# Performance work log

Measured on AMD Instinct MI355X. Metric: run time of the kernel, lower is better.

Reference implementation:

```python
import jax, jax.numpy as jnp
import numpy as np
from jax import lax

DG = 8          # deformable groups
KH = KW = 3
K = KH * KW
PAD = 1


def conv3x3(x, w, b):
    # x: (B,C,H,W), w: (O,C,3,3) -> SAME conv, stride 1
    y = lax.conv_general_dilated(x, w, (1, 1), ((PAD, PAD), (PAD, PAD)),
                                 dimension_numbers=('NCHW', 'OIHW', 'NCHW'))
    return y + b[None, :, None, None]


def lrelu(x):
    return jnp.where(x >= 0, x, 0.1 * x)


def modulated_deform_conv(x, offset, mask, w, b):
    """DCNv2 semantics: stride=1, pad=1, dilation=1, groups=1.
    x: (B,C,H,W); offset: (B, 2*DG*K, H, W); mask: (B, DG*K, H, W) (already sigmoided);
    w: (O, C, 3, 3); b: (O,).
    Offset channel layout per CUDA kernel: (DG, K, 2[y,x]).
    """
    B, C, H, W = x.shape
    cg = C // DG
    off = offset.reshape(B, DG, K, 2, H, W)
    dy, dx = off[:, :, :, 0], off[:, :, :, 1]            # (B,DG,K,H,W)

    ky, kx = jnp.meshgrid(jnp.arange(KH), jnp.arange(KW), indexing='ij')
    ky = ky.reshape(K).astype(x.dtype)
    kx = kx.reshape(K).astype(x.dtype)
    base_y = jnp.arange(H, dtype=x.dtype)[None, :, None] - PAD + ky[:, None, None]  # (K,H,1)
    base_x = jnp.arange(W, dtype=x.dtype)[None, None, :] - PAD + kx[:, None, None]  # (K,1,W)
    py = dy + base_y                                     # (B,DG,K,H,W)
    px = dx + base_x

    y0 = jnp.floor(py)
    x0 = jnp.floor(px)
    wy = py - y0
    wx = px - x0
    y0i = y0.astype(jnp.int32)
    x0i = x0.astype(jnp.int32)

    xg = x.reshape(B, DG, cg, H * W)

    def gather(yi, xi):
        valid = ((yi >= 0) & (yi < H) & (xi >= 0) & (xi < W)).astype(x.dtype)
        idx = jnp.clip(yi, 0, H - 1) * W + jnp.clip(xi, 0, W - 1)   # (B,DG,K,H,W)
        idxf = idx.reshape(B, DG, 1, K * H * W)
        vals = jnp.take_along_axis(xg, jnp.broadcast_to(idxf, (B, DG, cg, K * H * W)), axis=3)
        return vals.reshape(B, DG, cg, K, H, W) * valid[:, :, None]

    samp = gather(y0i, x0i) * ((1 - wy) * (1 - wx))[:, :, None]
    samp = samp + gather(y0i, x0i + 1) * ((1 - wy) * wx)[:, :, None]
    samp = samp + gather(y0i + 1, x0i) * (wy * (1 - wx))[:, :, None]
    samp = samp + gather(y0i + 1, x0i + 1) * (wy * wx)[:, :, None]

    samp = samp * mask.reshape(B, DG, 1, K, H, W)        # modulated
    wr = w.reshape(w.shape[0], DG, cg, K)
    out = jnp.einsum('odck,bdckhw->bohw', wr, samp)
    return out + b[None, :, None, None]


def dcn_pack(x, feat, off_w, off_b, w, b):
    # conv_offset on `feat` -> (B, 3*DG*K, H, W); chunk into o1,o2,mask
    out = conv3x3(feat, off_w, off_b)
    o1, o2, m = jnp.split(out, 3, axis=1)
    offset = jnp.concatenate([o1, o2], axis=1)
    mask = jax.nn.sigmoid(m)
    return modulated_deform_conv(x, offset, mask, w, b)


def setup_inputs() -> dict:
    key = jax.random.key(0)
    ks = jax.random.split(key, 24)
    B, C, H, W = 4, 64, 192, 192
    nf = C

    def wconv(k, o, i, s=0.02):
        return jax.random.normal(k, (o, i, 3, 3), jnp.float32) * s

    inp = {
        'nbr_l1': jax.random.normal(ks[0], (B, C, H, W), jnp.float32),
        'ref_l1': jax.random.normal(ks[1], (B, C, H, W), jnp.float32),
        'oc1_w': wconv(ks[2], nf, 2 * nf), 'oc1_b': jnp.zeros((nf,), jnp.float32),
        'oc2_w': wconv(ks[3], nf, nf), 'oc2_b': jnp.zeros((nf,), jnp.float32),
        'dcn1_off_w': wconv(ks[4], 3 * DG * K, nf, 0.01), 'dcn1_off_b': jnp.zeros((3 * DG * K,), jnp.float32),
        'dcn1_w': wconv(ks[5], nf, nf), 'dcn1_b': jnp.zeros((nf,), jnp.float32),
        'fc_w': wconv(ks[6], nf, nf), 'fc_b': jnp.zeros((nf,), jnp.float32),
        'cas1_w': wconv(ks[7], nf, 2 * nf), 'cas1_b': jnp.zeros((nf,), jnp.float32),
        'cas2_w': wconv(ks[8], nf, nf), 'cas2_b': jnp.zeros((nf,), jnp.float32),
        'casd_off_w': wconv(ks[9], 3 * DG * K, nf, 0.01), 'casd_off_b': jnp.zeros((3 * DG * K,), jnp.float32),
        'casd_w': wconv(ks[10], nf, nf), 'casd_b': jnp.zeros((nf,), jnp.float32),
    }
    return inp


def reference(nbr_l1, ref_l1, oc1_w, oc1_b, oc2_w, oc2_b,
              dcn1_off_w, dcn1_off_b, dcn1_w, dcn1_b, fc_w, fc_b,
              cas1_w, cas1_b, cas2_w, cas2_b,
              casd_off_w, casd_off_b, casd_w, casd_b):
    offset = jnp.concatenate([nbr_l1, ref_l1], axis=1)
    offset = lrelu(conv3x3(offset, oc1_w, oc1_b))
    offset = lrelu(conv3x3(offset, oc2_w, oc2_b))
    feat = dcn_pack(nbr_l1, offset, dcn1_off_w, dcn1_off_b, dcn1_w, dcn1_b)
    feat = conv3x3(feat, fc_w, fc_b)                     # no activation (matches source)
    offset = jnp.concatenate([feat, ref_l1], axis=1)
    offset = lrelu(conv3x3(lrelu(conv3x3(offset, cas1_w, cas1_b)), cas2_w, cas2_b))
    feat = lrelu(dcn_pack(feat, offset, casd_off_w, casd_off_b, casd_w, casd_b))
    return feat
```

## Files before the change

### kernel.cpp

```cpp
#include <hip/hip_runtime.h>
#include <hip/hip_bf16.h>
#include <math.h>

typedef __hip_bfloat16 bf16;
typedef float  floatx16 __attribute__((ext_vector_type(16)));
typedef short  short8   __attribute__((ext_vector_type(8)));

#define Bn 4
#define NF 64
#define Hn 192
#define Wn 192
#define HWn (Hn*Wn)

#define WA_OC1  0
#define WA_OC2  73728
#define WA_FC   110592
#define WA_CAS1 147456
#define WA_CAS2 221184
#define WA_D1O  258048
#define WA_CDO  405504
#define WP_D1   552960
#define WP_CD   589824
#define B_OC1  0
#define B_OC2  64
#define B_FC   128
#define B_CAS1 192
#define B_CAS2 256
#define B_D1O  320
#define B_CDO  536
#define B_D1P  752
#define B_CDP  816
#define BIAS_OFF  1024
#define WPOOL_OFF 5120
#define BUF_OFF   1261568
#define FEAT_BYTES 18874368

#define WROWS 12
#define WCOLS 12
#define WSTR  72
#define SSTR2 152

__device__ __forceinline__ float b2f(bf16 v){ return __bfloat162float(v); }
__device__ __forceinline__ bf16  f2b(float v){ return __float2bfloat16(v); }
__device__ __forceinline__ float us2f(unsigned short u){ return __uint_as_float(((unsigned)u) << 16); }
__device__ __forceinline__ float ld(const void* p, size_t i, int f32){
    if (f32) return ((const float*)p)[i];
    return b2f(((const bf16*)p)[i]);
}

union B8 { uint2 u2[2]; uint4 u4; short8 s8; };
union V8 { uint4 u4; unsigned short us[8]; bf16 h[8]; };
union V4 { uint2 u2; bf16 h[4]; };

struct P20 { const void* p[20]; int n[20]; };

__global__ void detect_bias(P20 a, int* __restrict__ flags, float* __restrict__ bp){
    __shared__ int sf[20];
    int t = threadIdx.x;
    if (t < 20){
        const unsigned short* u = (const unsigned short*)a.p[t];
        int n = a.n[t]; if (n > 512) n = 512;
        int f32 = 0;
        for (int i = 0; i < n; ++i){
            float v = __uint_as_float(((unsigned)u[i]) << 16);
            if (!(fabsf(v) < 1e3f)) f32 = 1;
        }
        sf[t] = f32; flags[t] = f32;
    }
    __syncthreads();
    const int src[9] = {3,5,11,13,15,7,17,9,19};
    const int off[9] = {B_OC1,B_OC2,B_FC,B_CAS1,B_CAS2,B_D1O,B_CDO,B_D1P,B_CDP};
    const int sz[9]  = {64,64,64,64,64,216,216,64,64};
    for (int s = 0; s < 9; ++s)
        if (t < sz[s]) bp[off[s] + t] = ld(a.p[src[s]], t, sf[src[s]]);
}

__global__ void prep_weights(P20 a, const int* __restrict__ flags, bf16* __restrict__ wp)
{
    const int srcI[9] = {2,4,10,12,14,6,16,8,18};
    const int dstO[9] = {WA_OC1,WA_OC2,WA_FC,WA_CAS1,WA_CAS2,WA_D1O,WA_CDO,WP_D1,WP_CD};
    const int cinA[9] = {128,64,64,128,64,64,64,0,0};
    const int coutA[9]= {64,64,64,64,64,216,216,0,0};
    const int nblk[9] = {288,144,144,288,144,576,576,144,144};

    int bx = blockIdx.x;
    int j = 0, base = 0;
    while (j < 8 && bx >= base + nblk[j]){ base += nblk[j]; ++j; }
    int idx = (bx - base)*256 + threadIdx.x;
    const void* src = a.p[srcI[j]];
    const int f = flags[srcI[j]];
    bf16* dst = wp + dstO[j];

    int jj = idx & 7;
    int ko = (idx>>3) & 1;
    int mm = (idx>>4) & 31;
    int rest = idx >> 9;
    if (cinA[j]){
        int KK = cinA[j] >> 4;
        int kk = rest % KK; rest /= KK;
        int tap = rest % 9;
        int ocb = rest / 9;
        int oc = ocb*32 + mm;
        int ci = kk*16 + ko*8 + jj;
        float v = 0.f;
        if (oc < coutA[j]) v = ld(src, ((size_t)oc*cinA[j] + ci)*9 + tap, f);
        dst[idx] = f2b(v);
    } else {
        int kk = rest % 36;
        int ocb = rest / 36;
        int oc = ocb*32 + mm;
        int kp   = kk*16 + ko*8 + jj;
        int slot = kp >> 3;
        int cg   = kp & 7;
        int dg   = slot / 9;
        int tap  = slot - dg*9;
        int k    = (dg*8 + cg)*9 + tap;
        dst[idx] = f2b(ld(src, (size_t)oc*576 + k, f));
    }
}

__global__ __launch_bounds__(256)
void pack_x(const void* __restrict__ src, const int* __restrict__ flags, int fi,
            bf16* __restrict__ dst)
{
    __shared__ bf16 s[64*65];
    const int b    = blockIdx.y;
    const int pix0 = blockIdx.x * 64;
    const int t    = threadIdx.x;
    const int f    = (fi >= 0) ? flags[fi] : 0;

    const int px8 = (t & 7) * 8;
    const int ci0 = t >> 3;
#pragma unroll
    for (int it = 0; it < 2; ++it){
        int ci = ci0 + it*32;
        size_t g = ((size_t)b*NF + ci)*HWn + pix0 + px8;
        if (f){
            float4 a0 = *(const float4*)((const float*)src + g);
            float4 a1 = *(const float4*)((const float*)src + g + 4);
            bf16* sp = &s[ci*65 + px8];
            sp[0]=f2b(a0.x); sp[1]=f2b(a0.y); sp[2]=f2b(a0.z); sp[3]=f2b(a0.w);
            sp[4]=f2b(a1.x); sp[5]=f2b(a1.y); sp[6]=f2b(a1.z); sp[7]=f2b(a1.w);
        } else {
            V8 v; v.u4 = *(const uint4*)((const bf16*)src + g);
            bf16* sp = &s[ci*65 + px8];
#pragma unroll
            for (int j = 0; j < 8; ++j) sp[j] = v.h[j];
        }
    }
    __syncthreads();

    const int px  = t >> 2;
    const int ch0 = (t & 3) * 16;
    V8 o0, o1;
#pragma unroll
    for (int j = 0; j < 8; ++j){
        o0.h[j] = s[(ch0 + j)*65 + px];
        o1.h[j] = s[(ch0 + 8 + j)*65 + px];
    }
    bf16* dp = dst + ((size_t)b*HWn + pix0 + px)*64 + ch0;
    *(uint4*)(dp)     = o0.u4;
    *(uint4*)(dp + 8) = o1.u4;
}

template<int KK, int NOCB>
__global__ __launch_bounds__(256)
void conv_mfma(const bf16* __restrict__ inA, const bf16* __restrict__ inB,
               const bf16* __restrict__ wA, const float* __restrict__ bias,
               bf16* __restrict__ out, int ACT)
{
    constexpr int CinT  = KK*16;
    constexpr int ciPad = CinT + 4;
    constexpr int CH8   = CinT/8;
    constexpr int CSH   = (KK==4)?3:4;
    extern __shared__ __align__(16) char smem_raw[];
    bf16* s_in = (bf16*)smem_raw;

    const int b  = blockIdx.z;
    const int bx = blockIdx.x;
    const int ty = bx/3, tx = bx - ty*3;
    const int h0 = ty*2, x0 = tx*64;
    const int tid = threadIdx.x;

    for (int r = 0; r < 4; ++r){
        const int y = h0 - 1 + r;
        const bool yv = (unsigned)y < (unsigned)Hn;
        const size_t rb = ((size_t)b*HWn + (size_t)y*Wn)*64;
        for (int e = tid; e < 66*CH8; e += 256){
            const int c   = e >> CSH;
            const int ch8 = e & (CH8-1);
            const int x = x0 - 1 + c;
            B8 v; v.u4 = make_uint4(0,0,0,0);
            if (yv && (unsigned)x < (unsigned)Wn){
                if (KK==8 && ch8 >= 8) v.u4 = *(const uint4*)(inB + rb + (size_t)x*64 + (ch8-8)*8);
                else                   v.u4 = *(const uint4*)(inA + rb + (size_t)x*64 + ch8*8);
            }
            bf16* dp = &s_in[(size_t)(r*66 + c)*ciPad + ch8*8];
            *(uint2*)(dp)     = v.u2[0];
            *(uint2*)(dp + 4) = v.u2[1];
        }
    }
    __syncthreads();

    const int w    = tid >> 6;
    const int lane = tid & 63;
    const int m    = lane & 31;
    const int half = lane >> 5;
    const int och  = (w >> 1) * 32;
    const int rw   = (w & 1);
    const int gpx0 = (h0 + rw)*Wn + x0;

#pragma unroll
    for (int ot = 0; ot < NOCB; ++ot){
        const int ocb = ot*2 + (w >> 1);
        const bf16* wb = wA + ((size_t)ocb*9*KK)*512 + m*16 + half*8;

        floatx16 a0, a1;
#pragma unroll
        for (int r = 0; r < 16; ++r){ a0[r] = 0.f; a1[r] = 0.f; }

        B8 ring[2][4];
#pragma unroll
        for (int i = 0; i < 4; ++i) ring[0][i].u4 = *(const uint4*)(wb + (size_t)i*512);

        constexpr int NCH = 9*KK/4;
#pragma unroll
        for (int tap = 0; tap < 9; ++tap){
            const int ky = tap/3, kx = tap - 3*(tap/3);
            const bf16* s0 = s_in + (size_t)((ky+rw)*66 + kx + m)*ciPad + half*8;
#pragma unroll
            for (int hh = 0; hh < KK/4; ++hh){
                const int cidx = tap*(KK/4) + hh;
                const int cur = cidx & 1, nxt = cur ^ 1;
                if (cidx + 1 < NCH){
#pragma unroll
                    for (int i = 0; i < 4; ++i)
                        ring[nxt][i].u4 = *(const uint4*)(wb + (size_t)((cidx+1)*4 + i)*512);
                }
#pragma unroll
                for (int i = 0; i < 4; ++i){
                    const bf16* p0 = s0 + hh*64 + i*16;
                    const bf16* p1 = p0 + 32*ciPad;
                    B8 b0, b1;
                    b0.u2[0] = *(const uint2*)(p0); b0.u2[1] = *(const uint2*)(p0+4);
                    b1.u2[0] = *(const uint2*)(p1); b1.u2[1] = *(const uint2*)(p1+4);
                    a0 = __builtin_amdgcn_mfma_f32_32x32x16_bf16(ring[cur][i].s8, b0.s8, a0, 0,0,0);
                    a1 = __builtin_amdgcn_mfma_f32_32x32x16_bf16(ring[cur][i].s8, b1.s8, a1, 0,0,0);
                }
            }
        }

        if (ACT == 2){
#pragma unroll
            for (int s = 0; s < 2; ++s){
                const int px = gpx0 + s*32 + m;
#pragma unroll
                for (int r = 0; r < 16; ++r){
                    int row = (r & 3) + 8*(r >> 2) + 4*half;
                    int oc  = ot*64 + och + row;
                    if (oc < 216){
                        float v = (s ? a1[r] : a0[r]) + bias[oc];
                        if (oc >= 144) v = 1.f/(1.f + __expf(-v));
                        out[((size_t)b*216 + oc)*HWn + px] = f2b(v);
                    }
                }
            }
        } else {
#pragma unroll
            for (int s = 0; s < 2; ++s){
                const int px = gpx0 + s*32 + m;
                bf16* ob = out + ((size_t)b*HWn + px)*64 + och + 4*half;
#pragma unroll
                for (int q = 0; q < 4; ++q){
                    V4 u;
#pragma unroll
                    for (int j = 0; j < 4; ++j){
                        float v = (s ? a1[q*4+j] : a0[q*4+j]) + bias[och + 4*half + 8*q + j];
                        if (ACT == 1) v = (v >= 0.f) ? v : 0.1f*v;
                        u.h[j] = f2b(v);
                    }
                    *(uint2*)(ob + 8*q) = u.u2;
                }
            }
        }
    }
}

__global__ __launch_bounds__(256)
void dcn_mfma(const bf16* __restrict__ xi,
              const bf16* __restrict__ offs,
              const bf16* __restrict__ wP,
              const float* __restrict__ pbias,
              void* __restrict__ out, int outF32, int ACT)
{
    __shared__ __align__(16) bf16 s_win[WROWS*WCOLS*WSTR];
    __shared__ __align__(16) bf16 s_samp[64*SSTR2];

    const int b   = blockIdx.y;
    const int bx  = blockIdx.x;
    const int tx  = bx % (Wn/8);
    const int ty  = bx / (Wn/8);
    const int gx0 = tx*8, gy0 = ty*8;
    const int wx0 = gx0 - 2, wy0 = gy0 - 2;
    const int tid = threadIdx.x;

    const bf16* xb = xi + (size_t)b*HWn*64;

    for (int c = tid; c < WROWS*WCOLS*8; c += 256){
        int ch4 = c & 7;
        int pxi = c >> 3;
        int gy  = wy0 + pxi/WCOLS;
        int gx  = wx0 + pxi%WCOLS;
        uint4 v = {0u,0u,0u,0u};
        if ((unsigned)gy < (unsigned)Hn && (unsigned)gx < (unsigned)Wn)
            v = *(const uint4*)(xb + ((size_t)gy*Wn + gx)*64 + ch4*8);
        *(uint4*)&s_win[pxi*WSTR + ch4*8] = v;
    }

    const int px   = tid & 63;
    const int wq   = tid >> 6;
    const int pr   = px >> 3, pc = px & 7;
    const int gy   = gy0 + pr, gx = gx0 + pc;
    const int m    = px & 31;
    const int half = px >> 5;
    const int och  = (wq >> 1) * 32;
    const int pxh  = (wq & 1) * 32;

    const size_t obase = (size_t)b*216*HWn + (size_t)gy*Wn + gx;
    const uint4 z4 = {0u,0u,0u,0u};

    const bf16* wPb  = wP + ((size_t)(wq>>1)*36)*512 + m*16 + half*8;
    const bf16* srow = s_samp + (pxh + m)*SSTR2 + half*8;

    floatx16 acc;
#pragma unroll
    for (int r = 0; r < 16; ++r) acc[r] = 0.f;

    for (int pass = 0; pass < 4; ++pass){
        __syncthreads();

#pragma unroll
        for (int ii = 0; ii < 5; ++ii){
            int sl = wq + ii*4;
            if (sl < 18){
                int dgl = sl / 9;
                int tap = sl - dgl*9;
                int dg  = pass*2 + dgl;
                int ky  = tap / 3;
                int kx  = tap - ky*3;
                float dy = b2f(offs[obase + (size_t)(dg*18 + tap*2    )*HWn]);
                float dx = b2f(offs[obase + (size_t)(dg*18 + tap*2 + 1)*HWn]);
                float mk = b2f(offs[obase + (size_t)(144 + dg*9 + tap )*HWn]);
                float py  = dy + (float)(gy - 1 + ky);
                float pxx = dx + (float)(gx - 1 + kx);
                float y0f = floorf(py), x0f = floorf(pxx);
                int   y0  = (int)y0f,   xi0 = (int)x0f;
                float wy  = py - y0f,   wx  = pxx - x0f;
                float w00 = (1.f-wy)*(1.f-wx)*mk, w01 = (1.f-wy)*wx*mk;
                float w10 = wy*(1.f-wx)*mk,       w11 = wy*wx*mk;
                int ly = y0 - wy0, lx = xi0 - wx0;

                auto fetch = [&](int ly_, int lx_, int y_, int x_) -> uint4 {
                    if ((unsigned)ly_ < (unsigned)WROWS && (unsigned)lx_ < (unsigned)WCOLS)
                        return *(const uint4*)&s_win[(ly_*WCOLS + lx_)*WSTR + dg*8];
                    if ((unsigned)y_ < (unsigned)Hn && (unsigned)x_ < (unsigned)Wn)
                        return *(const uint4*)(xb + ((size_t)y_*Wn + x_)*64 + dg*8);
                    return z4;
                };
                V8 c00, c01, c10, c11, o;
                c00.u4 = fetch(ly,   lx,   y0,   xi0  );
                c01.u4 = fetch(ly,   lx+1, y0,   xi0+1);
                c10.u4 = fetch(ly+1, lx,   y0+1, xi0  );
                c11.u4 = fetch(ly+1, lx+1, y0+1, xi0+1);
#pragma unroll
                for (int j = 0; j < 8; ++j){
                    float v = w00*us2f(c00.us[j]) + w01*us2f(c01.us[j])
                            + w10*us2f(c10.us[j]) + w11*us2f(c11.us[j]);
                    o.h[j] = f2b(v);
                }
                *(uint4*)&s_samp[px*SSTR2 + sl*8] = o.u4;
            }
        }
        __syncthreads();

#pragma unroll
        for (int kk = 0; kk < 9; ++kk){
            B8 ba; ba.u4 = *(const uint4*)(wPb + (size_t)(pass*9 + kk)*512);
            B8 bb; bb.u4 = *(const uint4*)(srow + kk*16);
            acc = __builtin_amdgcn_mfma_f32_32x32x16_bf16(ba.s8, bb.s8, acc, 0, 0, 0);
        }
    }

    const int opx = pxh + m;
    const int pxo = (gy0 + (opx >> 3))*Wn + gx0 + (opx & 7);
    if (outF32){
#pragma unroll
        for (int r = 0; r < 16; ++r){
            int row = (r & 3) + 8*(r >> 2) + 4*half;
            int oc  = och + row;
            float v = acc[r] + pbias[oc];
            if (ACT) v = (v >= 0.f) ? v : 0.1f*v;
            ((float*)out)[((size_t)b*NF + oc)*HWn + pxo] = v;
        }
    } else {
        bf16* ob = (bf16*)out + ((size_t)b*HWn + pxo)*64 + och + 4*half;
#pragma unroll
        for (int q = 0; q < 4; ++q){
            V4 u;
#pragma unroll
            for (int j = 0; j < 4; ++j){
                int oc = och + 4*half + 8*q + j;
                float v = acc[q*4 + j] + pbias[oc];
                if (ACT) v = (v >= 0.f) ? v : 0.1f*v;
                u.h[j] = f2b(v);
            }
            *(uint2*)(ob + 8*q) = u.u2;
        }
    }
}

extern "C" void kernel_launch(void* const* d_in, const int* in_sizes, int n_in,
                              void* d_out, int out_size, void* d_ws, size_t ws_size,
                              hipStream_t stream)
{
    enum { I_NBR=0, I_REF=1 };

    int*   flags = (int*)d_ws;
    float* bp    = (float*)((char*)d_ws + BIAS_OFF);
    bf16*  wp    = (bf16*) ((char*)d_ws + WPOOL_OFF);
    bf16*  t1    = (bf16*) ((char*)d_ws + BUF_OFF);
    bf16*  f1    = (bf16*) ((char*)d_ws + BUF_OFF + FEAT_BYTES);
    bf16*  offs  = (bf16*) ((char*)d_ws + BUF_OFF + 2*(size_t)FEAT_BYTES);
    bf16*  t0    = (bf16*) d_out;
    bf16*  nbr_i = (bf16*)((char*)d_out + FEAT_BYTES);
    bf16*  refA  = offs;
    bf16*  refB  = nbr_i;

    P20 a;
    for (int i = 0; i < 20; ++i){ a.p[i] = d_in[i]; a.n[i] = in_sizes[i]; }

    detect_bias<<<1, 256, 0, stream>>>(a, flags, bp);
    prep_weights<<<2448, 256, 0, stream>>>(a, flags, wp);

    dim3 blk(256,1,1);
    const int smem64  = 4*66*68*2;
    const int smem128 = 4*66*132*2;
    dim3 gC (288, 1, Bn);
    dim3 gD (576, Bn, 1);
    dim3 gP (576, Bn, 1);

    pack_x<<<gP, blk, 0, stream>>>(d_in[I_NBR], flags, I_NBR, nbr_i);
    pack_x<<<gP, blk, 0, stream>>>(d_in[I_REF], flags, I_REF, refA);
    conv_mfma<8,1><<<gC, blk, smem128, stream>>>(nbr_i, refA, wp+WA_OC1, bp+B_OC1, t0, 1);
    conv_mfma<4,1><<<gC, blk, smem64, stream>>>(t0, nullptr, wp+WA_OC2, bp+B_OC2, t1, 1);
    conv_mfma<4,4><<<gC, blk, smem64, stream>>>(t1, nullptr, wp+WA_D1O, bp+B_D1O, offs, 2);
    dcn_mfma<<<gD, blk, 0, stream>>>(nbr_i, offs, wp+WP_D1, bp+B_D1P, t1, 0, 0);
    pack_x<<<gP, blk, 0, stream>>>(d_in[I_REF], flags, I_REF, refB);
    conv_mfma<4,1><<<gC, blk, smem64, stream>>>(t1, nullptr, wp+WA_FC, bp+B_FC, f1, 0);
    conv_mfma<8,1><<<gC, blk, smem128, stream>>>(f1, refB, wp+WA_CAS1, bp+B_CAS1, t0, 1);
    conv_mfma<4,1><<<gC, blk, smem64, stream>>>(t0, nullptr, wp+WA_CAS2, bp+B_CAS2, t1, 1);
    conv_mfma<4,4><<<gC, blk, smem64, stream>>>(t1, nullptr, wp+WA_CDO, bp+B_CDO, offs, 2);
    dcn_mfma<<<gD, blk, 0, stream>>>(f1, offs, wp+WP_CD, bp+B_CDP, d_out, 1, 1);
}
```

Baseline: 862.3 us.

## Process four output rows per block in 64-channel convs to reuse weights

Adds a ROWS template parameter to the MFMA conv kernel so the 64-input-channel convolutions handle 4 output rows per block instead of 2, with each wave keeping 4 accumulators. Each weight fragment loaded from global memory is now reused across twice as many pixel sub-tiles, and the halo overhead in the staged input shrinks relative to output. The cost is more accumulator registers (64 floats), larger shared memory, half as many blocks, and the outer output-tile loop is no longer forced to unroll.

```diff
diff --git a/kernel.cpp b/kernel.cpp
--- a/kernel.cpp
+++ b/kernel.cpp
@@ -163,7 +163,7 @@
     *(uint4*)(dp + 8) = o1.u4;
 }
 
-template<int KK, int NOCB>
+template<int KK, int NOCB, int ROWS>
 __global__ __launch_bounds__(256)
 void conv_mfma(const bf16* __restrict__ inA, const bf16* __restrict__ inB,
                const bf16* __restrict__ wA, const float* __restrict__ bias,
@@ -173,16 +173,17 @@
     constexpr int ciPad = CinT + 4;
     constexpr int CH8   = CinT/8;
     constexpr int CSH   = (KK==4)?3:4;
+    constexpr int NSUB  = ROWS;
     extern __shared__ __align__(16) char smem_raw[];
     bf16* s_in = (bf16*)smem_raw;
 
     const int b  = blockIdx.z;
     const int bx = blockIdx.x;
     const int ty = bx/3, tx = bx - ty*3;
-    const int h0 = ty*2, x0 = tx*64;
+    const int h0 = ty*ROWS, x0 = tx*64;
     const int tid = threadIdx.x;
 
-    for (int r = 0; r < 4; ++r){
+    for (int r = 0; r < ROWS+2; ++r){
         const int y = h0 - 1 + r;
         const bool yv = (unsigned)y < (unsigned)Hn;
         const size_t rb = ((size_t)b*HWn + (size_t)y*Wn)*64;
@@ -207,17 +208,17 @@
     const int m    = lane & 31;
     const int half = lane >> 5;
     const int och  = (w >> 1) * 32;
-    const int rw   = (w & 1);
-    const int gpx0 = (h0 + rw)*Wn + x0;
-
-#pragma unroll
+    const int rwb  = (w & 1) * (ROWS/2);
+
     for (int ot = 0; ot < NOCB; ++ot){
         const int ocb = ot*2 + (w >> 1);
         const bf16* wb = wA + ((size_t)ocb*9*KK)*512 + m*16 + half*8;
 
-        floatx16 a0, a1;
-#pragma unroll
-        for (int r = 0; r < 16; ++r){ a0[r] = 0.f; a1[r] = 0.f; }
+        floatx16 acc[NSUB];
+#pragma unroll
+        for (int s = 0; s < NSUB; ++s)
+#pragma unroll
+            for (int r = 0; r < 16; ++r) acc[s][r] = 0.f;
 
         B8 ring[2][4];
 #pragma unroll
@@ -227,7 +228,6 @@
 #pragma unroll
         for (int tap = 0; tap < 9; ++tap){
             const int ky = tap/3, kx = tap - 3*(tap/3);
-            const bf16* s0 = s_in + (size_t)((ky+rw)*66 + kx + m)*ciPad + half*8;
 #pragma unroll
             for (int hh = 0; hh < KK/4; ++hh){
                 const int cidx = tap*(KK/4) + hh;
@@ -239,27 +239,34 @@
                 }
 #pragma unroll
                 for (int i = 0; i < 4; ++i){
-                    const bf16* p0 = s0 + hh*64 + i*16;
-                    const bf16* p1 = p0 + 32*ciPad;
-                    B8 b0, b1;
-                    b0.u2[0] = *(const uint2*)(p0); b0.u2[1] = *(const uint2*)(p0+4);
-                    b1.u2[0] = *(const uint2*)(p1); b1.u2[1] = *(const uint2*)(p1+4);
-                    a0 = __builtin_amdgcn_mfma_f32_32x32x16_bf16(ring[cur][i].s8, b0.s8, a0, 0,0,0);
-                    a1 = __builtin_amdgcn_mfma_f32_32x32x16_bf16(ring[cur][i].s8, b1.s8, a1, 0,0,0);
+#pragma unroll
+                    for (int s = 0; s < NSUB; ++s){
+                        const int ro  = (ROWS==4) ? (s>>1) : 0;
+                        const int pxh = (ROWS==4) ? (s&1)  : s;
+                        const bf16* p = s_in
+                            + (size_t)((ky + rwb + ro)*66 + kx + pxh*32 + m)*ciPad
+                            + half*8 + hh*64 + i*16;
+                        B8 bf;
+                        bf.u2[0] = *(const uint2*)(p);
+                        bf.u2[1] = *(const uint2*)(p + 4);
+                        acc[s] = __builtin_amdgcn_mfma_f32_32x32x16_bf16(ring[cur][i].s8, bf.s8, acc[s], 0,0,0);
+                    }
                 }
             }
         }
 
         if (ACT == 2){
 #pragma unroll
-            for (int s = 0; s < 2; ++s){
-                const int px = gpx0 + s*32 + m;
+            for (int s = 0; s < NSUB; ++s){
+                const int ro  = (ROWS==4) ? (s>>1) : 0;
+                const int pxh = (ROWS==4) ? (s&1)  : s;
+                const int px = (h0 + rwb + ro)*Wn + x0 + pxh*32 + m;
 #pragma unroll
                 for (int r = 0; r < 16; ++r){
                     int row = (r & 3) + 8*(r >> 2) + 4*half;
                     int oc  = ot*64 + och + row;
                     if (oc < 216){
-                        float v = (s ? a1[r] : a0[r]) + bias[oc];
+                        float v = acc[s][r] + bias[oc];
                         if (oc >= 144) v = 1.f/(1.f + __expf(-v));
                         out[((size_t)b*216 + oc)*HWn + px] = f2b(v);
                     }
@@ -267,15 +274,17 @@
             }
         } else {
 #pragma unroll
-            for (int s = 0; s < 2; ++s){
-                const int px = gpx0 + s*32 + m;
+            for (int s = 0; s < NSUB; ++s){
+                const int ro  = (ROWS==4) ? (s>>1) : 0;
+                const int pxh = (ROWS==4) ? (s&1)  : s;
+                const int px = (h0 + rwb + ro)*Wn + x0 + pxh*32 + m;
                 bf16* ob = out + ((size_t)b*HWn + px)*64 + och + 4*half;
 #pragma unroll
                 for (int q = 0; q < 4; ++q){
                     V4 u;
 #pragma unroll
                     for (int j = 0; j < 4; ++j){
-                        float v = (s ? a1[q*4+j] : a0[q*4+j]) + bias[och + 4*half + 8*q + j];
+                        float v = acc[s][q*4+j] + bias[och + 4*half + 8*q + j];
                         if (ACT == 1) v = (v >= 0.f) ? v : 0.1f*v;
                         u.h[j] = f2b(v);
                     }
@@ -443,22 +452,23 @@
     prep_weights<<<2448, 256, 0, stream>>>(a, flags, wp);
 
     dim3 blk(256,1,1);
-    const int smem64  = 4*66*68*2;
+    const int smem4r = 6*66*68*2;
     const int smem128 = 4*66*132*2;
-    dim3 gC (288, 1, Bn);
+    dim3 gC4 (144, 1, Bn);
+    dim3 gC8 (288, 1, Bn);
     dim3 gD (576, Bn, 1);
     dim3 gP (576, Bn, 1);
 
     pack_x<<<gP, blk, 0, stream>>>(d_in[I_NBR], flags, I_NBR, nbr_i);
     pack_x<<<gP, blk, 0, stream>>>(d_in[I_REF], flags, I_REF, refA);
-    conv_mfma<8,1><<<gC, blk, smem128, stream>>>(nbr_i, refA, wp+WA_OC1, bp+B_OC1, t0, 1);
-    conv_mfma<4,1><<<gC, blk, smem64, stream>>>(t0, nullptr, wp+WA_OC2, bp+B_OC2, t1, 1);
-    conv_mfma<4,4><<<gC, blk, smem64, stream>>>(t1, nullptr, wp+WA_D1O, bp+B_D1O, offs, 2);
+    conv_mfma<8,1,2><<<gC8, blk, smem128, stream>>>(nbr_i, refA, wp+WA_OC1, bp+B_OC1, t0, 1);
+    conv_mfma<4,1,4><<<gC4, blk, smem4r, stream>>>(t0, nullptr, wp+WA_OC2, bp+B_OC2, t1, 1);
+    conv_mfma<4,4,4><<<gC4, blk, smem4r, stream>>>(t1, nullptr, wp+WA_D1O, bp+B_D1O, offs, 2);
     dcn_mfma<<<gD, blk, 0, stream>>>(nbr_i, offs, wp+WP_D1, bp+B_D1P, t1, 0, 0);
     pack_x<<<gP, blk, 0, stream>>>(d_in[I_REF], flags, I_REF, refB);
-    conv_mfma<4,1><<<gC, blk, smem64, stream>>>(t1, nullptr, wp+WA_FC, bp+B_FC, f1, 0);
-    conv_mfma<8,1><<<gC, blk, smem128, stream>>>(f1, refB, wp+WA_CAS1, bp+B_CAS1, t0, 1);
-    conv_mfma<4,1><<<gC, blk, smem64, stream>>>(t0, nullptr, wp+WA_CAS2, bp+B_CAS2, t1, 1);
-    conv_mfma<4,4><<<gC, blk, smem64, stream>>>(t1, nullptr, wp+WA_CDO, bp+B_CDO, offs, 2);
+    conv_mfma<4,1,4><<<gC4, blk, smem4r, stream>>>(t1, nullptr, wp+WA_FC, bp+B_FC, f1, 0);
+    conv_mfma<8,1,2><<<gC8, blk, smem128, stream>>>(f1, refB, wp+WA_CAS1, bp+B_CAS1, t0, 1);
+    conv_mfma<4,1,4><<<gC4, blk, smem4r, stream>>>(t0, nullptr, wp+WA_CAS2, bp+B_CAS2, t1, 1);
+    conv_mfma<4,4,4><<<gC4, blk, smem4r, stream>>>(t1, nullptr, wp+WA_CDO, bp+B_CDO, offs, 2);
     dcn_mfma<<<gD, blk, 0, stream>>>(f1, offs, wp+WP_CD, bp+B_CDP, d_out, 1, 1);
 }
```

New measurement: 943.4 us. 9.4% more time.
